# Kernel optimization log

Measured on AMD Instinct MI355X. Metric: run time of the kernel, lower is better.

The kernel has to match this reference:

```python
import jax, jax.numpy as jnp
import numpy as np

NEG_SLOPE = 0.2  # PyG GATConv default negative_slope
HEADS1, HID = 8, 256


def gat_conv(x, src, dst, W, att_src, att_dst, bias, heads, out_ch):
    """PyG-style GATConv: project, per-edge attention, segment softmax over dst, scatter-add."""
    N = x.shape[0]
    h = (x @ W.T).reshape(N, heads, out_ch)                 # [N,H,C]
    a_s = jnp.einsum('nhc,hc->nh', h, att_src)              # [N,H]
    a_d = jnp.einsum('nhc,hc->nh', h, att_dst)
    e = jax.nn.leaky_relu(a_s[src] + a_d[dst], NEG_SLOPE)   # [E,H]
    m = jax.ops.segment_max(e, dst, num_segments=N)         # stable softmax per dst node
    ex = jnp.exp(e - m[dst])
    denom = jax.ops.segment_sum(ex, dst, num_segments=N)
    alpha = ex / (denom[dst] + 1e-16)                       # [E,H]
    out = jax.ops.segment_sum(alpha[:, :, None] * h[src], dst, num_segments=N)  # [N,H,C]
    return out.reshape(N, heads * out_ch) + bias


def setup_inputs() -> dict:
    key = jax.random.key(0)
    ks = jax.random.split(key, 20)
    Nc, Ncol, E = 4000, 16000, 100000
    nf, cf, gain, hid, H, emb = 64, 128, 2, HID, HEADS1, 128
    s = 0.05
    return {
        'constraints_state': jax.random.normal(ks[0], (Nc, nf), jnp.float32),
        'columns_state':     jax.random.normal(ks[1], (Ncol, cf), jnp.float32),
        'edges':             jax.random.randint(ks[2], (2, E), 0, Nc + Ncol, jnp.int64),
        'W_node': jax.random.normal(ks[3], (hid, nf * gain), jnp.float32) * s,
        'b_node': jnp.zeros((hid,), jnp.float32),
        'W_col':  jax.random.normal(ks[4], (hid, cf * gain), jnp.float32) * s,
        'b_col':  jnp.zeros((hid,), jnp.float32),
        'W1':       jax.random.normal(ks[5], (H * hid, hid), jnp.float32) * s,
        'att_src1': jax.random.normal(ks[6], (H, hid), jnp.float32) * s,
        'att_dst1': jax.random.normal(ks[7], (H, hid), jnp.float32) * s,
        'b1':       jnp.zeros((H * hid,), jnp.float32),
        'W2':       jax.random.normal(ks[8], (hid, H * hid), jnp.float32) * s,
        'att_src2': jax.random.normal(ks[9], (1, hid), jnp.float32) * s,
        'att_dst2': jax.random.normal(ks[10], (1, hid), jnp.float32) * s,
        'b2':       jnp.zeros((hid,), jnp.float32),
        'W_out': jax.random.normal(ks[11], (emb, hid), jnp.float32) * s,
        'b_out': jnp.zeros((emb,), jnp.float32),
    }


def reference(constraints_state, columns_state, edges,
              W_node, b_node, W_col, b_col,
              W1, att_src1, att_dst1, b1,
              W2, att_src2, att_dst2, b2,
              W_out, b_out):
    gain = 2
    x_n = jnp.tile(constraints_state, (1, gain))
    x_c = jnp.tile(columns_state, (1, gain))
    h_n = jax.nn.relu(x_n @ W_node.T + b_node)
    h_c = jax.nn.relu(x_c @ W_col.T + b_col)
    x = jnp.concatenate([h_n, h_c], axis=0)                 # [N, hid]
    N = x.shape[0]
    loops = jnp.arange(N)
    # conv1: edges as given (+ self-loops, PyG default)
    src1 = jnp.concatenate([edges[0], loops])
    dst1 = jnp.concatenate([edges[1], loops])
    x = jax.nn.relu(gat_conv(x, src1, dst1, W1, att_src1, att_dst1, b1, HEADS1, HID))
    # conv2: flipped edges (+ self-loops), 1 head
    src2 = jnp.concatenate([edges[1], loops])
    dst2 = jnp.concatenate([edges[0], loops])
    x = jax.nn.relu(gat_conv(x, src2, dst2, W2, att_src2, att_dst2, b2, 1, HID))
    logits = x[-columns_state.shape[0]:] @ W_out.T + b_out  # [Ncol, embed_dim]
    return logits
```

## Files before the change

### kernel.cpp

```cpp
#include <hip/hip_runtime.h>


#define NEG_SLOPE 0.2f

typedef __attribute__((ext_vector_type(8))) short bf16x8;
typedef __attribute__((ext_vector_type(4))) float f32x4;

__device__ __forceinline__ float bf2f(unsigned short u) {
  return __uint_as_float(((unsigned)u) << 16);
}
__device__ __forceinline__ unsigned short f2bf(float f) {
  unsigned u = __float_as_uint(f);
  u += 0x7fffu + ((u >> 16) & 1u);
  return (unsigned short)(u >> 16);
}

__device__ __forceinline__ void async_copy16(const void* g, void* l) {
  __builtin_amdgcn_global_load_lds(
      (const __attribute__((address_space(1))) unsigned int*)g,
      (__attribute__((address_space(3))) unsigned int*)l, 16, 0, 0);
}

__global__ void prep(const float* __restrict__ Wn, const float* __restrict__ Wc,
                     const float* __restrict__ W1, const float* __restrict__ W2,
                     const float* __restrict__ Wout,
                     const float* __restrict__ cons, const float* __restrict__ cols,
                     const float* __restrict__ att_s1, const float* __restrict__ att_d1,
                     unsigned short* __restrict__ Wn_b, unsigned short* __restrict__ Wc_b,
                     unsigned short* __restrict__ W1b, unsigned short* __restrict__ W2b,
                     unsigned short* __restrict__ Woutb,
                     unsigned short* __restrict__ consb, unsigned short* __restrict__ colsb,
                     float* __restrict__ v_s1, float* __restrict__ v_d1,
                     int n_cons, int n_cols) {
  const int S0 = 256 * 64;
  const int S1 = 256 * 128;
  const int S2 = 2048 * 256;
  const int S3 = 256 * 2048;
  const int S4 = 128 * 256;
  const int S5 = 2048;
  int total = S0 + S1 + S2 + S3 + S4 + n_cons + n_cols + S5;
  for (int idx = blockIdx.x * 256 + threadIdx.x; idx < total; idx += gridDim.x * 256) {
    int i = idx;
    if (i < S0) { int o = i >> 6, j = i & 63;
      Wn_b[i] = f2bf(Wn[o * 128 + j] + Wn[o * 128 + 64 + j]); continue; }
    i -= S0;
    if (i < S1) { int o = i >> 7, j = i & 127;
      Wc_b[i] = f2bf(Wc[o * 256 + j] + Wc[o * 256 + 128 + j]); continue; }
    i -= S1;
    if (i < S2) { W1b[i] = f2bf(W1[i]); continue; }
    i -= S2;
    if (i < S3) { W2b[i] = f2bf(W2[i]); continue; }
    i -= S3;
    if (i < S4) { Woutb[i] = f2bf(Wout[i]); continue; }
    i -= S4;
    if (i < n_cons) { consb[i] = f2bf(cons[i]); continue; }
    i -= n_cons;
    if (i < n_cols) { colsb[i] = f2bf(cols[i]); continue; }
    i -= n_cols;
    {
      int h = i >> 8, k = i & 255;
      const float* Wrow = W1 + (size_t)h * 256 * 256 + k;
      const float* as = att_s1 + h * 256;
      const float* ad = att_d1 + h * 256;
      float s = 0.f, d = 0.f;
      for (int c = 0; c < 256; ++c) {
        float w = Wrow[(size_t)c * 256];
        s += as[c] * w;
        d += ad[c] * w;
      }
      v_s1[i] = s; v_d1[i] = d;
    }
  }
}

__global__ __launch_bounds__(256) void a1_dots(const unsigned short* __restrict__ xb,
                                               const float* __restrict__ v_s,
                                               const float* __restrict__ v_d,
                                               float* __restrict__ a_s,
                                               float* __restrict__ a_d, int N) {
  __shared__ float vs[2048], vd[2048];
  for (int i = threadIdx.x; i < 2048; i += 256) { vs[i] = v_s[i]; vd[i] = v_d[i]; }
  __syncthreads();
  int n = blockIdx.x * 256 + threadIdx.x;
  if (n >= N) return;
  const unsigned short* row = xb + (size_t)n * 256;
  float s[8] = {}, d[8] = {};
  for (int c = 0; c < 256; c += 8) {
    bf16x8 xv = *(const bf16x8*)(row + c);
    float xf[8];
#pragma unroll
    for (int i = 0; i < 8; ++i) xf[i] = bf2f(((const unsigned short*)&xv)[i]);
#pragma unroll
    for (int h = 0; h < 8; ++h)
#pragma unroll
      for (int i = 0; i < 8; ++i) {
        s[h] += xf[i] * vs[h * 256 + c + i];
        d[h] += xf[i] * vd[h * 256 + c + i];
      }
  }
#pragma unroll
  for (int h = 0; h < 8; ++h) { a_s[n * 8 + h] = s[h]; a_d[n * 8 + h] = d[h]; }
}

__global__ __launch_bounds__(256) void a2_dots(const unsigned short* __restrict__ h2,
                                               const float* __restrict__ att_s,
                                               const float* __restrict__ att_d,
                                               float* __restrict__ a_s,
                                               float* __restrict__ a_d, int N) {
  __shared__ float ss[256], sd[256];
  if (threadIdx.x < 256) {
    ss[threadIdx.x] = att_s[threadIdx.x];
    sd[threadIdx.x] = att_d[threadIdx.x];
  }
  __syncthreads();
  int n = blockIdx.x * 256 + threadIdx.x;
  if (n >= N) return;
  const unsigned short* row = h2 + (size_t)n * 256;
  float s = 0.f, d = 0.f;
  for (int c = 0; c < 256; c += 8) {
    bf16x8 xv = *(const bf16x8*)(row + c);
#pragma unroll
    for (int i = 0; i < 8; ++i) {
      float hv = bf2f(((const unsigned short*)&xv)[i]);
      s += hv * ss[c + i];
      d += hv * sd[c + i];
    }
  }
  a_s[n] = s;
  a_d[n] = d;
}

template <bool C_BF16, bool BIAS, bool RELU, bool BDIAG>
__global__ __launch_bounds__(512) void gemm_mfma_bt(const unsigned short* __restrict__ A,
                                                    const unsigned short* __restrict__ W,
                                                    const float* __restrict__ bias,
                                                    void* __restrict__ Cv,
                                                    int M, int K, int Nout, int lda) {
  __shared__ short smem[2 * 128 * 64];
  short* sA = smem;
  short* sB = smem + 128 * 64;
  float* Cf = (float*)Cv;
  unsigned short* Cb = (unsigned short*)Cv;

  const int tid = threadIdx.x;
  const int lane = tid & 63, w = tid >> 6;
  const int m0 = blockIdx.y * 128, n0 = blockIdx.x * 128;
  const int koff = BDIAG ? (n0 >> 8) << 8 : 0;
  const int wm = (w & 3) * 32, wn = (w >> 2) * 64;
  const int fr = lane & 15;
  const int frs = fr & 7;
  const int quad = lane >> 4;

  f32x4 acc[2][4];
#pragma unroll
  for (int i = 0; i < 2; ++i)
#pragma unroll
    for (int j = 0; j < 4; ++j) acc[i][j] = (f32x4){0.f, 0.f, 0.f, 0.f};

  for (int k0 = 0; k0 < K; k0 += 64) {
#pragma unroll
    for (int i = 0; i < 2; ++i) {
      int c = i * 512 + tid;
      int row = c >> 3, kc = c & 7;
      int kcs = kc ^ (row & 7);
      int grow = m0 + row;
      if (grow >= M) grow = M - 1;
      async_copy16(A + (size_t)grow * lda + koff + k0 + kcs * 8, &sA[(i * 512 + w * 64) * 8]);
    }
#pragma unroll
    for (int i = 0; i < 2; ++i) {
      int c = i * 512 + tid;
      int row = c >> 3, kc = c & 7;
      int kcs = kc ^ (row & 7);
      async_copy16(W + (size_t)(n0 + row) * K + k0 + kcs * 8, &sB[(i * 512 + w * 64) * 8]);
    }
    __syncthreads();

#pragma unroll
    for (int ks = 0; ks < 2; ++ks) {
      bf16x8 af[2], bfr[4];
#pragma unroll
      for (int mi = 0; mi < 2; ++mi) {
        int row = wm + mi * 16 + fr;
        af[mi] = *(const bf16x8*)&sA[(row * 8 + ((ks * 4 + quad) ^ frs)) * 8];
      }
#pragma unroll
      for (int ni = 0; ni < 4; ++ni) {
        int row = wn + ni * 16 + fr;
        bfr[ni] = *(const bf16x8*)&sB[(row * 8 + ((ks * 4 + quad) ^ frs)) * 8];
      }
#pragma unroll
      for (int mi = 0; mi < 2; ++mi)
#pragma unroll
        for (int ni = 0; ni < 4; ++ni)
          acc[mi][ni] = __builtin_amdgcn_mfma_f32_16x16x32_bf16(
              af[mi], bfr[ni], acc[mi][ni], 0, 0, 0);
    }
    __syncthreads();
  }

  if (C_BF16) {
    unsigned short* hsh = (unsigned short*)smem;
#pragma unroll
    for (int mi = 0; mi < 2; ++mi)
#pragma unroll
      for (int ni = 0; ni < 4; ++ni) {
        int col = wn + ni * 16 + fr;
        float bv = BIAS ? bias[n0 + col] : 0.f;
        f32x4 v = acc[mi][ni];
#pragma unroll
        for (int r = 0; r < 4; ++r) {
          int row = wm + mi * 16 + quad * 4 + r;
          float x = v[r] + bv;
          if (RELU) x = fmaxf(x, 0.f);
          hsh[row * 128 + (col ^ (((row >> 2) & 3) << 5))] = f2bf(x);
        }
      }
    __syncthreads();
#pragma unroll
    for (int i = 0; i < 4; ++i) {
      int slot = i * 512 + tid;
      int row = slot >> 4, cg = slot & 15;
      int colbase = cg * 8;
      bf16x8 val = *(const bf16x8*)&hsh[row * 128 + (colbase ^ (((row >> 2) & 3) << 5))];
      int grow = m0 + row;
      if (grow < M)
        *(bf16x8*)(Cb + (size_t)grow * Nout + n0 + colbase) = val;
    }
  } else {
#pragma unroll
    for (int mi = 0; mi < 2; ++mi)
#pragma unroll
      for (int ni = 0; ni < 4; ++ni) {
        int col = n0 + wn + ni * 16 + fr;
        float bv = BIAS ? bias[col] : 0.f;
        f32x4 v = acc[mi][ni];
#pragma unroll
        for (int r = 0; r < 4; ++r) {
          int row = m0 + wm + mi * 16 + quad * 4 + r;
          if (row < M) {
            float x = v[r] + bv;
            if (RELU) x = fmaxf(x, 0.f);
            Cf[(size_t)row * Nout + col] = x;
          }
        }
      }
  }
}

__global__ void build_count(const void* __restrict__ edges_raw, int E, int N,
                            int* __restrict__ esrc, int* __restrict__ edst,
                            int* __restrict__ cnt1, int* __restrict__ cnt2, int E1) {
  const long long* p64 = (const long long*)edges_raw;
  const int* p32 = (const int*)edges_raw;
  bool is64 = true;
#pragma unroll
  for (int i = 0; i < 8; ++i) {
    long long v = p64[i];
    if (v < 0 || v >= N) is64 = false;
  }
  int idx = blockIdx.x * 256 + threadIdx.x;
  if (idx >= E1) return;
  int s, d;
  if (idx < E) {
    if (is64) { s = (int)p64[idx]; d = (int)p64[E + idx]; }
    else      { s = p32[idx];      d = p32[E + idx]; }
  } else {
    s = d = idx - E;
  }
  esrc[idx] = s;
  edst[idx] = d;
  atomicAdd(&cnt1[d], 1);
  atomicAdd(&cnt2[s], 1);
}

__device__ __forceinline__ void scan_one(const int* __restrict__ cnt,
                                         int* __restrict__ indptr,
                                         int* __restrict__ cur, int N, int* buf) {
  int t = threadIdx.x, lane = t & 63, w = t >> 6;
  int running = 0;
  for (int base = 0; base < N; base += 1024) {
    int v = (base + t < N) ? cnt[base + t] : 0;
    int incl = v;
#pragma unroll
    for (int off = 1; off < 64; off <<= 1) {
      int y = __shfl_up(incl, off);
      if (lane >= off) incl += y;
    }
    if (lane == 63) buf[w] = incl;
    __syncthreads();
    if (t < 16) {
      int x = buf[t];
#pragma unroll
      for (int off = 1; off < 16; off <<= 1) {
        int y = __shfl_up(x, off);
        if (t >= off) x += y;
      }
      buf[t] = x;
    }
    __syncthreads();
    int woff = w ? buf[w - 1] : 0;
    int tot = buf[15];
    if (base + t < N) {
      int excl = running + woff + incl - v;
      indptr[base + t] = excl;
      cur[base + t] = excl;
    }
    running += tot;
    __syncthreads();
  }
  if (t == 0) indptr[N] = running;
  __syncthreads();
}

__global__ __launch_bounds__(1024) void scan2_kernel(const int* cnt1, int* indptr1, int* cur1,
                                                     const int* cnt2, int* indptr2, int* cur2,
                                                     int N) {
  __shared__ int buf[16];
  scan_one(cnt1, indptr1, cur1, N, buf);
  scan_one(cnt2, indptr2, cur2, N, buf);
}

__global__ void scatter_edges(const int* __restrict__ esrc, const int* __restrict__ edst,
                              int* __restrict__ cur1, int* __restrict__ cur2,
                              int* __restrict__ nbr1, int* __restrict__ nbr2, int E1) {
  int e = blockIdx.x * 256 + threadIdx.x;
  if (e >= E1) return;
  int s = esrc[e], d = edst[e];
  int p1 = atomicAdd(&cur1[d], 1);
  nbr1[p1] = s;
  int p2 = atomicAdd(&cur2[s], 1);
  nbr2[p2] = d;
}

__global__ __launch_bounds__(256) void alpha1_kernel(const float* __restrict__ a_s,
                                                     const float* __restrict__ a_d,
                                                     const int* __restrict__ indptr,
                                                     const int* __restrict__ nbr,
                                                     float* __restrict__ alpha, int N) {
  int n = blockIdx.x * 256 + threadIdx.x;
  if (n >= N) return;
  int start = indptr[n], end = indptr[n + 1];
  float ad[8];
  *(float4*)&ad[0] = *(const float4*)&a_d[n * 8];
  *(float4*)&ad[4] = *(const float4*)&a_d[n * 8 + 4];
  float m[8], ssum[8];
#pragma unroll
  for (int h = 0; h < 8; ++h) { m[h] = -1e30f; ssum[h] = 0.f; }
  for (int p = start; p < end; ++p) {
    int s = nbr[p];
    float as[8];
    *(float4*)&as[0] = *(const float4*)&a_s[s * 8];
    *(float4*)&as[4] = *(const float4*)&a_s[s * 8 + 4];
#pragma unroll
    for (int h = 0; h < 8; ++h) {
      float e = as[h] + ad[h];
      e = e > 0.f ? e : NEG_SLOPE * e;
      float nm = fmaxf(m[h], e);
      ssum[h] = ssum[h] * __expf(m[h] - nm) + __expf(e - nm);
      m[h] = nm;
    }
  }
  float inv[8];
#pragma unroll
  for (int h = 0; h < 8; ++h) inv[h] = 1.f / (ssum[h] + 1e-16f);
  for (int p = start; p < end; ++p) {
    int s = nbr[p];
    float as[8];
    *(float4*)&as[0] = *(const float4*)&a_s[s * 8];
    *(float4*)&as[4] = *(const float4*)&a_s[s * 8 + 4];
    float av[8];
#pragma unroll
    for (int h = 0; h < 8; ++h) {
      float e = as[h] + ad[h];
      e = e > 0.f ? e : NEG_SLOPE * e;
      av[h] = __expf(e - m[h]) * inv[h];
    }
    *(float4*)&alpha[(size_t)p * 8] = *(const float4*)&av[0];
    *(float4*)&alpha[(size_t)p * 8 + 4] = *(const float4*)&av[4];
  }
}

__global__ __launch_bounds__(256) void agg1_kernel(const unsigned short* __restrict__ xb,
                                                   const float* __restrict__ alpha,
                                                   const int* __restrict__ indptr,
                                                   const int* __restrict__ nbr,
                                                   unsigned short* __restrict__ agg,
                                                   int N) {
  __shared__ float al_sh[4][64 * 8];
  const int w = threadIdx.x >> 6, lane = threadIdx.x & 63;
  const int dst = blockIdx.x * 4 + w;
  if (dst >= N) return;
  const int start = indptr[dst];
  const int deg = indptr[dst + 1] - start;
  const int c0 = lane * 4;

  float acc[8][4];
#pragma unroll
  for (int h = 0; h < 8; ++h)
#pragma unroll
    for (int i = 0; i < 4; ++i) acc[h][i] = 0.f;

  for (int base = 0; base < deg; base += 64) {
    int cnt = min(64, deg - base);
    int s = 0;
    if (lane < cnt) {
      int slot = start + base + lane;
      s = nbr[slot];
      f32x4 a0 = *(const f32x4*)&alpha[(size_t)slot * 8];
      f32x4 a1 = *(const f32x4*)&alpha[(size_t)slot * 8 + 4];
      *(f32x4*)&al_sh[w][lane * 8] = a0;
      *(f32x4*)&al_sh[w][lane * 8 + 4] = a1;
    }
    __builtin_amdgcn_wave_barrier();
    for (int j = 0; j < cnt; ++j) {
      int sj = __shfl(s, j);
      f32x4 alo = *(const f32x4*)&al_sh[w][j * 8];
      f32x4 ahi = *(const f32x4*)&al_sh[w][j * 8 + 4];
      ushort4 xv = *(const ushort4*)(xb + (size_t)sj * 256 + c0);
      float x0 = bf2f(xv.x), x1 = bf2f(xv.y), x2 = bf2f(xv.z), x3 = bf2f(xv.w);
#pragma unroll
      for (int h = 0; h < 4; ++h) {
        acc[h][0] += alo[h] * x0; acc[h][1] += alo[h] * x1;
        acc[h][2] += alo[h] * x2; acc[h][3] += alo[h] * x3;
      }
#pragma unroll
      for (int h = 0; h < 4; ++h) {
        acc[h + 4][0] += ahi[h] * x0; acc[h + 4][1] += ahi[h] * x1;
        acc[h + 4][2] += ahi[h] * x2; acc[h + 4][3] += ahi[h] * x3;
      }
    }
    __builtin_amdgcn_wave_barrier();
  }

  unsigned short* op = agg + (size_t)dst * 2048;
#pragma unroll
  for (int h = 0; h < 8; ++h) {
    unsigned short ov[4];
#pragma unroll
    for (int i = 0; i < 4; ++i) ov[i] = f2bf(acc[h][i]);
    *((ushort4*)(op + h * 256 + c0)) = *((const ushort4*)ov);
  }
}

__global__ __launch_bounds__(256) void agg2_fused(const unsigned short* __restrict__ h2,
                                                  const float* __restrict__ a_s,
                                                  const float* __restrict__ a_d,
                                                  const int* __restrict__ indptr,
                                                  const int* __restrict__ nbr,
                                                  const float* __restrict__ b2,
                                                  unsigned short* __restrict__ x3,
                                                  int Nc, int Ncol) {
  const int w = threadIdx.x >> 6, lane = threadIdx.x & 63;
  const int i0 = blockIdx.x * 4 + w;
  if (i0 >= Ncol) return;
  const int dst = Nc + i0;
  const int start = indptr[dst];
  const int deg = indptr[dst + 1] - start;
  const float ad = a_d[dst];
  float run_m = -1e30f, run_s = 0.f;
  float acc[4] = {0.f, 0.f, 0.f, 0.f};
  const int c0 = lane * 4;

  for (int base = 0; base < deg; base += 64) {
    int cnt = min(64, deg - base);
    float ev = -1e30f;
    int s = 0;
    if (lane < cnt) {
      s = nbr[start + base + lane];
      float e = a_s[s] + ad;
      ev = e > 0.f ? e : NEG_SLOPE * e;
    }
    float cm = ev;
#pragma unroll
    for (int off = 32; off; off >>= 1) cm = fmaxf(cm, __shfl_xor(cm, off));
    float nm = fmaxf(run_m, cm);
    float sc = __expf(run_m - nm);
    float e = (lane < cnt) ? __expf(ev - nm) : 0.f;
    float cs = e;
#pragma unroll
    for (int off = 32; off; off >>= 1) cs += __shfl_xor(cs, off);
    run_s = run_s * sc + cs;
    run_m = nm;
#pragma unroll
    for (int i = 0; i < 4; ++i) acc[i] *= sc;
    for (int j = 0; j < cnt; ++j) {
      int sj = __shfl(s, j);
      float al = __shfl(e, j);
      ushort4 hv = *(const ushort4*)(h2 + (size_t)sj * 256 + c0);
      acc[0] += al * bf2f(hv.x);
      acc[1] += al * bf2f(hv.y);
      acc[2] += al * bf2f(hv.z);
      acc[3] += al * bf2f(hv.w);
    }
  }

  float inv = 1.f / (run_s + 1e-16f);
  float4 bv = *(const float4*)&b2[c0];
  unsigned short ov[4];
  ov[0] = f2bf(fmaxf(acc[0] * inv + bv.x, 0.f));
  ov[1] = f2bf(fmaxf(acc[1] * inv + bv.y, 0.f));
  ov[2] = f2bf(fmaxf(acc[2] * inv + bv.z, 0.f));
  ov[3] = f2bf(fmaxf(acc[3] * inv + bv.w, 0.f));
  *((ushort4*)(x3 + (size_t)i0 * 256 + c0)) = *((const ushort4*)ov);
}

extern "C" void kernel_launch(void* const* d_in, const int* in_sizes, int n_in,
                              void* d_out, int out_size, void* d_ws, size_t ws_size,
                              hipStream_t stream) {
  (void)n_in; (void)out_size; (void)ws_size;
  const float* constraints = (const float*)d_in[0];
  const float* columns     = (const float*)d_in[1];
  const void*  edges       = d_in[2];
  const float* W_node = (const float*)d_in[3];
  const float* b_node = (const float*)d_in[4];
  const float* W_col  = (const float*)d_in[5];
  const float* b_col  = (const float*)d_in[6];
  const float* W1       = (const float*)d_in[7];
  const float* att_src1 = (const float*)d_in[8];
  const float* att_dst1 = (const float*)d_in[9];
  const float* b1       = (const float*)d_in[10];
  const float* W2       = (const float*)d_in[11];
  const float* att_src2 = (const float*)d_in[12];
  const float* att_dst2 = (const float*)d_in[13];
  const float* b2       = (const float*)d_in[14];
  const float* W_out    = (const float*)d_in[15];
  const float* b_out    = (const float*)d_in[16];

  const int Nc   = in_sizes[0] / 64;
  const int Ncol = in_sizes[1] / 128;
  const int E    = in_sizes[2] / 2;
  const int N    = Nc + Ncol;
  const int E1   = E + N;

  char* p = (char*)d_ws;
  size_t off = 0;
  auto alloc = [&](size_t nbytes) -> void* {
    void* r = p + off;
    off = (off + nbytes + 255) & ~(size_t)255;
    return r;
  };
  unsigned short* Wn_b  = (unsigned short*)alloc(2ull * 256 * 64);
  unsigned short* Wc_b  = (unsigned short*)alloc(2ull * 256 * 128);
  unsigned short* W1b   = (unsigned short*)alloc(2ull * 2048 * 256);
  unsigned short* W2b   = (unsigned short*)alloc(2ull * 256 * 2048);
  unsigned short* Woutb = (unsigned short*)alloc(2ull * 128 * 256);
  unsigned short* consb = (unsigned short*)alloc(2ull * (size_t)Nc * 64);
  unsigned short* colsb = (unsigned short*)alloc(2ull * (size_t)Ncol * 128);
  unsigned short* xb    = (unsigned short*)alloc(2ull * (size_t)N * 256);
  float* v_s1 = (float*)alloc(sizeof(float) * 8 * 256);
  float* v_d1 = (float*)alloc(sizeof(float) * 8 * 256);
  float* a_s1 = (float*)alloc(sizeof(float) * (size_t)N * 8);
  float* a_d1 = (float*)alloc(sizeof(float) * (size_t)N * 8);
  int* esrc = (int*)alloc(4ull * E1);
  int* edst = (int*)alloc(4ull * E1);
  int* cnt1 = (int*)alloc(4ull * 2 * N);
  int* cnt2 = cnt1 + N;
  int* indptr1 = (int*)alloc(4ull * (N + 1));
  int* cur1    = (int*)alloc(4ull * N);
  int* indptr2 = (int*)alloc(4ull * (N + 1));
  int* cur2    = (int*)alloc(4ull * N);
  int* nbr1 = (int*)alloc(4ull * E1);
  int* nbr2 = (int*)alloc(4ull * E1);
  float* alpha1 = (float*)alloc(sizeof(float) * 8ull * E1);
  unsigned short* agg = (unsigned short*)alloc(2ull * (size_t)N * 2048);
  unsigned short* x2  = (unsigned short*)alloc(2ull * (size_t)N * 2048);
  unsigned short* h2b = (unsigned short*)alloc(2ull * (size_t)N * 256);
  float* a_s2 = (float*)alloc(sizeof(float) * (size_t)N);
  float* a_d2 = (float*)alloc(sizeof(float) * (size_t)N);
  unsigned short* x3 = (unsigned short*)alloc(2ull * (size_t)Ncol * 256);

  hipMemsetAsync(cnt1, 0, 4ull * 2 * N, stream);
  prep<<<1024, 256, 0, stream>>>(W_node, W_col, W1, W2, W_out, constraints, columns,
                                 att_src1, att_dst1,
                                 Wn_b, Wc_b, W1b, W2b, Woutb, consb, colsb,
                                 v_s1, v_d1, Nc * 64, Ncol * 128);

  gemm_mfma_bt<true, true, true, false><<<dim3(2, (Nc + 127) / 128), 512, 0, stream>>>(
      consb, Wn_b, b_node, xb, Nc, 64, 256, 64);
  gemm_mfma_bt<true, true, true, false><<<dim3(2, (Ncol + 127) / 128), 512, 0, stream>>>(
      colsb, Wc_b, b_col, xb + (size_t)Nc * 256, Ncol, 128, 256, 128);

  a1_dots<<<(N + 255) / 256, 256, 0, stream>>>(xb, v_s1, v_d1, a_s1, a_d1, N);

  build_count<<<(E1 + 255) / 256, 256, 0, stream>>>(edges, E, N, esrc, edst, cnt1, cnt2, E1);
  scan2_kernel<<<1, 1024, 0, stream>>>(cnt1, indptr1, cur1, cnt2, indptr2, cur2, N);
  scatter_edges<<<(E1 + 255) / 256, 256, 0, stream>>>(esrc, edst, cur1, cur2, nbr1, nbr2, E1);

  alpha1_kernel<<<(N + 255) / 256, 256, 0, stream>>>(a_s1, a_d1, indptr1, nbr1, alpha1, N);
  agg1_kernel<<<(N + 3) / 4, 256, 0, stream>>>(xb, alpha1, indptr1, nbr1, agg, N);
  gemm_mfma_bt<true, true, true, true><<<dim3(16, (N + 127) / 128), 512, 0, stream>>>(
      agg, W1b, b1, x2, N, 256, 2048, 2048);

  gemm_mfma_bt<true, false, false, false><<<dim3(2, (N + 127) / 128), 512, 0, stream>>>(
      x2, W2b, nullptr, h2b, N, 2048, 256, 2048);
  a2_dots<<<(N + 255) / 256, 256, 0, stream>>>(h2b, att_src2, att_dst2, a_s2, a_d2, N);
  agg2_fused<<<(Ncol + 3) / 4, 256, 0, stream>>>(h2b, a_s2, a_d2, indptr2, nbr2, b2, x3,
                                                 Nc, Ncol);

  gemm_mfma_bt<false, true, false, false><<<dim3(1, (Ncol + 127) / 128), 512, 0, stream>>>(
      x3, Woutb, b_out, (float*)d_out, Ncol, 256, 128, 256);
}
```

Baseline: 370.8 us.

## Widen W1 GEMM tile to 256 columns and remap blocks across XCDs

Templatizes the MFMA GEMM on an N-tile multiplier so the conv1 projection uses 128x256 tiles, each covering a full head. This reuses the A tile across twice as many output columns. It also remaps workgroup IDs so that consecutive tiles land on the same XCD, for better L2 locality. The cost is higher register and LDS use per block and fewer blocks in the grid.

Result: no change. 377.3 us (+1.8%).

```diff
diff --git a/kernel.cpp b/kernel.cpp
--- a/kernel.cpp
+++ b/kernel.cpp
@@ -130,13 +130,13 @@
   a_d[n] = d;
 }
 
-template <bool C_BF16, bool BIAS, bool RELU, bool BDIAG>
+template <bool C_BF16, bool BIAS, bool RELU, bool BDIAG, int NI>
 __global__ __launch_bounds__(512) void gemm_mfma_bt(const unsigned short* __restrict__ A,
                                                     const unsigned short* __restrict__ W,
                                                     const float* __restrict__ bias,
                                                     void* __restrict__ Cv,
                                                     int M, int K, int Nout, int lda) {
-  __shared__ short smem[2 * 128 * 64];
+  __shared__ short smem[128 * 64 + NI * 128 * 64];
   short* sA = smem;
   short* sB = smem + 128 * 64;
   float* Cf = (float*)Cv;
@@ -144,18 +144,26 @@
 
   const int tid = threadIdx.x;
   const int lane = tid & 63, w = tid >> 6;
-  const int m0 = blockIdx.y * 128, n0 = blockIdx.x * 128;
+
+  const int gx = gridDim.x;
+  const int nwg = gx * gridDim.y;
+  int orig = blockIdx.y * gx + blockIdx.x;
+  int q = nwg >> 3, r = nwg & 7;
+  int xcd = orig & 7, idx = orig >> 3;
+  int wg = (xcd < r ? xcd * (q + 1) : r * (q + 1) + (xcd - r) * q) + idx;
+  const int m0 = (wg / gx) * 128, n0 = (wg % gx) * (128 * NI);
+
   const int koff = BDIAG ? (n0 >> 8) << 8 : 0;
   const int wm = (w & 3) * 32, wn = (w >> 2) * 64;
   const int fr = lane & 15;
   const int frs = fr & 7;
   const int quad = lane >> 4;
 
-  f32x4 acc[2][4];
+  f32x4 acc[2][4 * NI];
 #pragma unroll
   for (int i = 0; i < 2; ++i)
 #pragma unroll
-    for (int j = 0; j < 4; ++j) acc[i][j] = (f32x4){0.f, 0.f, 0.f, 0.f};
+    for (int j = 0; j < 4 * NI; ++j) acc[i][j] = (f32x4){0.f, 0.f, 0.f, 0.f};
 
   for (int k0 = 0; k0 < K; k0 += 64) {
 #pragma unroll
@@ -168,7 +176,7 @@
       async_copy16(A + (size_t)grow * lda + koff + k0 + kcs * 8, &sA[(i * 512 + w * 64) * 8]);
     }
 #pragma unroll
-    for (int i = 0; i < 2; ++i) {
+    for (int i = 0; i < 2 * NI; ++i) {
       int c = i * 512 + tid;
       int row = c >> 3, kc = c & 7;
       int kcs = kc ^ (row & 7);
@@ -178,21 +186,21 @@
 
 #pragma unroll
     for (int ks = 0; ks < 2; ++ks) {
-      bf16x8 af[2], bfr[4];
+      bf16x8 af[2], bfr[4 * NI];
 #pragma unroll
       for (int mi = 0; mi < 2; ++mi) {
         int row = wm + mi * 16 + fr;
         af[mi] = *(const bf16x8*)&sA[(row * 8 + ((ks * 4 + quad) ^ frs)) * 8];
       }
 #pragma unroll
-      for (int ni = 0; ni < 4; ++ni) {
-        int row = wn + ni * 16 + fr;
+      for (int ni = 0; ni < 4 * NI; ++ni) {
+        int row = wn + (ni & 3) * 16 + (ni >> 2) * 128 + fr;
         bfr[ni] = *(const bf16x8*)&sB[(row * 8 + ((ks * 4 + quad) ^ frs)) * 8];
       }
 #pragma unroll
       for (int mi = 0; mi < 2; ++mi)
 #pragma unroll
-        for (int ni = 0; ni < 4; ++ni)
+        for (int ni = 0; ni < 4 * NI; ++ni)
           acc[mi][ni] = __builtin_amdgcn_mfma_f32_16x16x32_bf16(
               af[mi], bfr[ni], acc[mi][ni], 0, 0, 0);
     }
@@ -202,44 +210,48 @@
   if (C_BF16) {
     unsigned short* hsh = (unsigned short*)smem;
 #pragma unroll
+    for (int nh = 0; nh < NI; ++nh) {
+#pragma unroll
+      for (int mi = 0; mi < 2; ++mi)
+#pragma unroll
+        for (int nl = 0; nl < 4; ++nl) {
+          int col = wn + nl * 16 + fr;
+          float bv = BIAS ? bias[n0 + nh * 128 + col] : 0.f;
+          f32x4 v = acc[mi][nh * 4 + nl];
+#pragma unroll
+          for (int rr = 0; rr < 4; ++rr) {
+            int row = wm + mi * 16 + quad * 4 + rr;
+            float x = v[rr] + bv;
+            if (RELU) x = fmaxf(x, 0.f);
+            hsh[row * 128 + (col ^ (((row >> 2) & 3) << 5))] = f2bf(x);
+          }
+        }
+      __syncthreads();
+#pragma unroll
+      for (int i = 0; i < 4; ++i) {
+        int slot = i * 512 + tid;
+        int row = slot >> 4, cg = slot & 15;
+        int colbase = cg * 8;
+        bf16x8 val = *(const bf16x8*)&hsh[row * 128 + (colbase ^ (((row >> 2) & 3) << 5))];
+        int grow = m0 + row;
+        if (grow < M)
+          *(bf16x8*)(Cb + (size_t)grow * Nout + n0 + nh * 128 + colbase) = val;
+      }
+      if (nh + 1 < NI) __syncthreads();
+    }
+  } else {
+#pragma unroll
     for (int mi = 0; mi < 2; ++mi)
 #pragma unroll
-      for (int ni = 0; ni < 4; ++ni) {
-        int col = wn + ni * 16 + fr;
-        float bv = BIAS ? bias[n0 + col] : 0.f;
-        f32x4 v = acc[mi][ni];
-#pragma unroll
-        for (int r = 0; r < 4; ++r) {
-          int row = wm + mi * 16 + quad * 4 + r;
-          float x = v[r] + bv;
-          if (RELU) x = fmaxf(x, 0.f);
-          hsh[row * 128 + (col ^ (((row >> 2) & 3) << 5))] = f2bf(x);
-        }
-      }
-    __syncthreads();
-#pragma unroll
-    for (int i = 0; i < 4; ++i) {
-      int slot = i * 512 + tid;
-      int row = slot >> 4, cg = slot & 15;
-      int colbase = cg * 8;
-      bf16x8 val = *(const bf16x8*)&hsh[row * 128 + (colbase ^ (((row >> 2) & 3) << 5))];
-      int grow = m0 + row;
-      if (grow < M)
-        *(bf16x8*)(Cb + (size_t)grow * Nout + n0 + colbase) = val;
-    }
-  } else {
-#pragma unroll
-    for (int mi = 0; mi < 2; ++mi)
-#pragma unroll
-      for (int ni = 0; ni < 4; ++ni) {
-        int col = n0 + wn + ni * 16 + fr;
+      for (int ni = 0; ni < 4 * NI; ++ni) {
+        int col = n0 + wn + (ni & 3) * 16 + (ni >> 2) * 128 + fr;
         float bv = BIAS ? bias[col] : 0.f;
         f32x4 v = acc[mi][ni];
 #pragma unroll
-        for (int r = 0; r < 4; ++r) {
-          int row = m0 + wm + mi * 16 + quad * 4 + r;
+        for (int rr = 0; rr < 4; ++rr) {
+          int row = m0 + wm + mi * 16 + quad * 4 + rr;
           if (row < M) {
-            float x = v[r] + bv;
+            float x = v[rr] + bv;
             if (RELU) x = fmaxf(x, 0.f);
             Cf[(size_t)row * Nout + col] = x;
           }
@@ -576,9 +588,9 @@
                                  Wn_b, Wc_b, W1b, W2b, Woutb, consb, colsb,
                                  v_s1, v_d1, Nc * 64, Ncol * 128);
 
-  gemm_mfma_bt<true, true, true, false><<<dim3(2, (Nc + 127) / 128), 512, 0, stream>>>(
+  gemm_mfma_bt<true, true, true, false, 1><<<dim3(2, (Nc + 127) / 128), 512, 0, stream>>>(
       consb, Wn_b, b_node, xb, Nc, 64, 256, 64);
-  gemm_mfma_bt<true, true, true, false><<<dim3(2, (Ncol + 127) / 128), 512, 0, stream>>>(
+  gemm_mfma_bt<true, true, true, false, 1><<<dim3(2, (Ncol + 127) / 128), 512, 0, stream>>>(
       colsb, Wc_b, b_col, xb + (size_t)Nc * 256, Ncol, 128, 256, 128);
 
   a1_dots<<<(N + 255) / 256, 256, 0, stream>>>(xb, v_s1, v_d1, a_s1, a_d1, N);
@@ -589,15 +601,15 @@
 
   alpha1_kernel<<<(N + 255) / 256, 256, 0, stream>>>(a_s1, a_d1, indptr1, nbr1, alpha1, N);
   agg1_kernel<<<(N + 3) / 4, 256, 0, stream>>>(xb, alpha1, indptr1, nbr1, agg, N);
-  gemm_mfma_bt<true, true, true, true><<<dim3(16, (N + 127) / 128), 512, 0, stream>>>(
+  gemm_mfma_bt<true, true, true, true, 2><<<dim3(8, (N + 127) / 128), 512, 0, stream>>>(
       agg, W1b, b1, x2, N, 256, 2048, 2048);
 
-  gemm_mfma_bt<true, false, false, false><<<dim3(2, (N + 127) / 128), 512, 0, stream>>>(
+  gemm_mfma_bt<true, false, false, false, 1><<<dim3(2, (N + 127) / 128), 512, 0, stream>>>(
       x2, W2b, nullptr, h2b, N, 2048, 256, 2048);
   a2_dots<<<(N + 255) / 256, 256, 0, stream>>>(h2b, att_src2, att_dst2, a_s2, a_d2, N);
   agg2_fused<<<(Ncol + 3) / 4, 256, 0, stream>>>(h2b, a_s2, a_d2, indptr2, nbr2, b2, x3,
                                                  Nc, Ncol);
 
-  gemm_mfma_bt<false, true, false, false><<<dim3(1, (Ncol + 127) / 128), 512, 0, stream>>>(
+  gemm_mfma_bt<false, true, false, false, 1><<<dim3(1, (Ncol + 127) / 128), 512, 0, stream>>>(
       x3, Woutb, b_out, (float*)d_out, Ncol, 256, 128, 256);
 }
```

## Fuse conv1 block-diagonal GEMM with conv2 projection to skip x2 round trip

Applied to the files above, without the earlier changes.

The new kernel computes each head's 256-wide conv1 output tile (bias plus ReLU) in shared memory and immediately multiplies it by the matching W2 slice, accumulating h2 in registers. This removes the N×2048 bf16 x2 intermediate write and read and one kernel launch. The generic GEMM also gets an XCD-aware block remapping for locality across chiplets. The fused kernel uses only about 157 blocks of 512 threads with heavy LDS and register use, so occupancy and parallelism are reduced.

After: 437.7 us. 18.1% more time.

```diff
diff --git a/kernel.cpp b/kernel.cpp
--- a/kernel.cpp
+++ b/kernel.cpp
@@ -130,7 +130,7 @@
   a_d[n] = d;
 }
 
-template <bool C_BF16, bool BIAS, bool RELU, bool BDIAG>
+template <bool C_BF16, bool BIAS, bool RELU>
 __global__ __launch_bounds__(512) void gemm_mfma_bt(const unsigned short* __restrict__ A,
                                                     const unsigned short* __restrict__ W,
                                                     const float* __restrict__ bias,
@@ -144,8 +144,15 @@
 
   const int tid = threadIdx.x;
   const int lane = tid & 63, w = tid >> 6;
-  const int m0 = blockIdx.y * 128, n0 = blockIdx.x * 128;
-  const int koff = BDIAG ? (n0 >> 8) << 8 : 0;
+
+  const int gx = gridDim.x;
+  const int nwg = gx * gridDim.y;
+  int orig = blockIdx.y * gx + blockIdx.x;
+  int q = nwg >> 3, r = nwg & 7;
+  int xcd = orig & 7, idx = orig >> 3;
+  int wg = (xcd < r ? xcd * (q + 1) : r * (q + 1) + (xcd - r) * q) + idx;
+  const int m0 = (wg / gx) * 128, n0 = (wg % gx) * 128;
+
   const int wm = (w & 3) * 32, wn = (w >> 2) * 64;
   const int fr = lane & 15;
   const int frs = fr & 7;
@@ -165,7 +172,7 @@
       int kcs = kc ^ (row & 7);
       int grow = m0 + row;
       if (grow >= M) grow = M - 1;
-      async_copy16(A + (size_t)grow * lda + koff + k0 + kcs * 8, &sA[(i * 512 + w * 64) * 8]);
+      async_copy16(A + (size_t)grow * lda + k0 + kcs * 8, &sA[(i * 512 + w * 64) * 8]);
     }
 #pragma unroll
     for (int i = 0; i < 2; ++i) {
@@ -245,6 +252,155 @@
           }
         }
       }
+  }
+}
+
+__global__ __launch_bounds__(512, 2) void conv12_fused(
+    const unsigned short* __restrict__ agg,
+    const unsigned short* __restrict__ W1,
+    const unsigned short* __restrict__ W2,
+    const float* __restrict__ b1,
+    unsigned short* __restrict__ h2,
+    int M) {
+  __shared__ short sAX[4 * 128 * 64];
+  __shared__ short sB[2][256 * 64];
+
+  const int tid = threadIdx.x;
+  const int lane = tid & 63, w = tid >> 6;
+  const int m0 = blockIdx.x * 128;
+  const int fr = lane & 15, quad = lane >> 4;
+  const int frs = fr & 7;
+  const int wm = (w & 3) * 32;
+  const int wc = (w >> 2) * 128;
+
+  f32x4 acc2[2][8];
+#pragma unroll
+  for (int i = 0; i < 2; ++i)
+#pragma unroll
+    for (int j = 0; j < 8; ++j) acc2[i][j] = (f32x4){0.f, 0.f, 0.f, 0.f};
+
+  auto STAGE_A = [&](int h) {
+#pragma unroll
+    for (int i = 0; i < 8; ++i) {
+      int c = i * 512 + tid;
+      int panel = c >> 10, cp = c & 1023;
+      int row = cp >> 3, kc = cp & 7;
+      int kcs = kc ^ (row & 7);
+      int grow = m0 + row;
+      if (grow >= M) grow = M - 1;
+      async_copy16(agg + (size_t)grow * 2048 + h * 256 + panel * 64 + kcs * 8,
+                   &sAX[(i * 512 + w * 64) * 8]);
+    }
+  };
+  auto STAGE_W1 = [&](int h, int k0, int b) {
+#pragma unroll
+    for (int i = 0; i < 4; ++i) {
+      int c = i * 512 + tid;
+      int row = c >> 3, kc = c & 7;
+      int kcs = kc ^ (row & 7);
+      async_copy16(W1 + (size_t)(h * 256 + row) * 256 + k0 + kcs * 8,
+                   &sB[b][(i * 512 + w * 64) * 8]);
+    }
+  };
+  auto STAGE_W2 = [&](int h, int k0, int b) {
+#pragma unroll
+    for (int i = 0; i < 4; ++i) {
+      int c = i * 512 + tid;
+      int row = c >> 3, kc = c & 7;
+      int kcs = kc ^ (row & 7);
+      async_copy16(W2 + (size_t)row * 2048 + h * 256 + k0 + kcs * 8,
+                   &sB[b][(i * 512 + w * 64) * 8]);
+    }
+  };
+  auto GSTEP = [&](int step, int b, f32x4 (*ac)[8]) {
+#pragma unroll
+    for (int ks = 0; ks < 2; ++ks) {
+      bf16x8 af[2], bfr[8];
+#pragma unroll
+      for (int mi = 0; mi < 2; ++mi) {
+        int row = wm + mi * 16 + fr;
+        af[mi] = *(const bf16x8*)
+            &sAX[((step * 128 + row) * 8 + ((ks * 4 + quad) ^ frs)) * 8];
+      }
+#pragma unroll
+      for (int ni = 0; ni < 8; ++ni) {
+        int row = wc + ni * 16 + fr;
+        bfr[ni] = *(const bf16x8*)
+            &sB[b][(row * 8 + ((ks * 4 + quad) ^ frs)) * 8];
+      }
+#pragma unroll
+      for (int mi = 0; mi < 2; ++mi)
+#pragma unroll
+        for (int ni = 0; ni < 8; ++ni)
+          ac[mi][ni] = __builtin_amdgcn_mfma_f32_16x16x32_bf16(
+              af[mi], bfr[ni], ac[mi][ni], 0, 0, 0);
+    }
+  };
+
+  for (int hh = 0; hh < 8; ++hh) {
+    f32x4 acc1[2][8];
+#pragma unroll
+    for (int i = 0; i < 2; ++i)
+#pragma unroll
+      for (int j = 0; j < 8; ++j) acc1[i][j] = (f32x4){0.f, 0.f, 0.f, 0.f};
+
+    STAGE_A(hh);
+    STAGE_W1(hh, 0, 0);
+    __syncthreads();
+#pragma unroll
+    for (int t = 0; t < 4; ++t) {
+      if (t < 3) STAGE_W1(hh, (t + 1) * 64, (t + 1) & 1);
+      else       STAGE_W2(hh, 0, 0);
+      GSTEP(t, t & 1, acc1);
+      __syncthreads();
+    }
+
+#pragma unroll
+    for (int mi = 0; mi < 2; ++mi)
+#pragma unroll
+      for (int ni = 0; ni < 8; ++ni) {
+        int col = wc + ni * 16 + fr;
+        float bv = b1[hh * 256 + col];
+        f32x4 v = acc1[mi][ni];
+#pragma unroll
+        for (int r = 0; r < 4; ++r) {
+          int row = wm + mi * 16 + quad * 4 + r;
+          float x = fmaxf(v[r] + bv, 0.f);
+          sAX[(((col >> 6) * 128 + row) * 8 +
+               (((col >> 3) & 7) ^ (row & 7))) * 8 + (col & 7)] = (short)f2bf(x);
+        }
+      }
+    __syncthreads();
+
+#pragma unroll
+    for (int t = 0; t < 4; ++t) {
+      if (t < 3) STAGE_W2(hh, (t + 1) * 64, (t + 1) & 1);
+      GSTEP(t, t & 1, acc2);
+      __syncthreads();
+    }
+  }
+
+  unsigned short* hsh = (unsigned short*)sAX;
+#pragma unroll
+  for (int mi = 0; mi < 2; ++mi)
+#pragma unroll
+    for (int ni = 0; ni < 8; ++ni) {
+      int col = wc + ni * 16 + fr;
+      f32x4 v = acc2[mi][ni];
+#pragma unroll
+      for (int r = 0; r < 4; ++r) {
+        int row = wm + mi * 16 + quad * 4 + r;
+        hsh[row * 256 + col] = f2bf(v[r]);
+      }
+    }
+  __syncthreads();
+#pragma unroll
+  for (int i = 0; i < 8; ++i) {
+    int slot = i * 512 + tid;
+    int row = slot >> 5, cg = slot & 31;
+    int grow = m0 + row;
+    if (grow < M)
+      *(bf16x8*)(h2 + (size_t)grow * 256 + cg * 8) = *(const bf16x8*)&hsh[row * 256 + cg * 8];
   }
 }
 
@@ -564,7 +720,6 @@
   int* nbr2 = (int*)alloc(4ull * E1);
   float* alpha1 = (float*)alloc(sizeof(float) * 8ull * E1);
   unsigned short* agg = (unsigned short*)alloc(2ull * (size_t)N * 2048);
-  unsigned short* x2  = (unsigned short*)alloc(2ull * (size_t)N * 2048);
   unsigned short* h2b = (unsigned short*)alloc(2ull * (size_t)N * 256);
   float* a_s2 = (float*)alloc(sizeof(float) * (size_t)N);
   float* a_d2 = (float*)alloc(sizeof(float) * (size_t)N);
@@ -576,9 +731,9 @@
                                  Wn_b, Wc_b, W1b, W2b, Woutb, consb, colsb,
                                  v_s1, v_d1, Nc * 64, Ncol * 128);
 
-  gemm_mfma_bt<true, true, true, false><<<dim3(2, (Nc + 127) / 128), 512, 0, stream>>>(
+  gemm_mfma_bt<true, true, true><<<dim3(2, (Nc + 127) / 128), 512, 0, stream>>>(
       consb, Wn_b, b_node, xb, Nc, 64, 256, 64);
-  gemm_mfma_bt<true, true, true, false><<<dim3(2, (Ncol + 127) / 128), 512, 0, stream>>>(
+  gemm_mfma_bt<true, true, true><<<dim3(2, (Ncol + 127) / 128), 512, 0, stream>>>(
       colsb, Wc_b, b_col, xb + (size_t)Nc * 256, Ncol, 128, 256, 128);
 
   a1_dots<<<(N + 255) / 256, 256, 0, stream>>>(xb, v_s1, v_d1, a_s1, a_d1, N);
@@ -589,15 +744,13 @@
 
   alpha1_kernel<<<(N + 255) / 256, 256, 0, stream>>>(a_s1, a_d1, indptr1, nbr1, alpha1, N);
   agg1_kernel<<<(N + 3) / 4, 256, 0, stream>>>(xb, alpha1, indptr1, nbr1, agg, N);
-  gemm_mfma_bt<true, true, true, true><<<dim3(16, (N + 127) / 128), 512, 0, stream>>>(
-      agg, W1b, b1, x2, N, 256, 2048, 2048);
-
-  gemm_mfma_bt<true, false, false, false><<<dim3(2, (N + 127) / 128), 512, 0, stream>>>(
-      x2, W2b, nullptr, h2b, N, 2048, 256, 2048);
+
+  conv12_fused<<<(N + 127) / 128, 512, 0, stream>>>(agg, W1b, W2b, b1, h2b, N);
+
   a2_dots<<<(N + 255) / 256, 256, 0, stream>>>(h2b, att_src2, att_dst2, a_s2, a_d2, N);
   agg2_fused<<<(Ncol + 3) / 4, 256, 0, stream>>>(h2b, a_s2, a_d2, indptr2, nbr2, b2, x3,
                                                  Nc, Ncol);
 
-  gemm_mfma_bt<false, true, false, false><<<dim3(1, (Ncol + 127) / 128), 512, 0, stream>>>(
+  gemm_mfma_bt<false, true, false><<<dim3(1, (Ncol + 127) / 128), 512, 0, stream>>>(
       x3, Woutb, b_out, (float*)d_out, Ncol, 256, 128, 256);
 }
```
